# Optimization experiments

Hardware: AMD Instinct MI355X
Metric: run time of the kernel (lower is better)

## Reference

```python
import jax, jax.numpy as jnp
import numpy as np

N, F, H, D = 4096, 512, 4, 64        # nodes, in features, heads, per-head dim
HID, OUT, NCLS, E = 1024, 256, 40, 65536  # FFN hidden, GAT dim, classes, edges
EPS = 1e-5


def _bn(x, g, b):
    # BatchNorm1d with batch statistics (training-mode math, biased variance)
    m = x.mean(axis=0)
    v = jnp.var(x, axis=0)
    return (x - m) * jax.lax.rsqrt(v + EPS) * g + b


def _ffn(x, g1, b1, W1, c1, g2, b2, W2, c2):
    x = jax.nn.gelu(_bn(x, g1, b1) @ W1.T + c1, approximate=False)
    x = jax.nn.gelu(_bn(x, g2, b2) @ W2.T + c2, approximate=False)
    return x


def setup_inputs() -> dict:
    key = jax.random.key(0)
    ks = jax.random.split(key, 12)
    nrm = lambda k, shape: jax.random.normal(k, shape, jnp.float32) * 0.05
    node_features = jax.random.normal(ks[0], (N, F), jnp.float32)
    edges = jax.random.randint(ks[1], (2, E), 0, N)
    adj = jnp.eye(N, dtype=bool)  # self loops, as in __init__
    adj = adj.at[edges[0], edges[1]].set(True)
    adj = adj.at[edges[1], edges[0]].set(True)
    return dict(
        node_features=node_features,
        pre_g1=jnp.ones(F), pre_b1=jnp.zeros(F),
        pre_W1=nrm(ks[2], (HID, F)), pre_c1=jnp.zeros(HID),
        pre_g2=jnp.ones(HID), pre_b2=jnp.zeros(HID),
        pre_W2=nrm(ks[3], (OUT, HID)), pre_c2=jnp.zeros(OUT),
        Wp=nrm(ks[4], (H * D, OUT)),           # GAT preprocess Linear, no bias
        Wa=nrm(ks[5], (2 * D,)),               # attention Linear(2d -> 1), no bias
        ln_g=jnp.ones(OUT), ln_b=jnp.zeros(OUT),
        post_g1=jnp.ones(OUT), post_b1=jnp.zeros(OUT),
        post_W1=nrm(ks[6], (HID, OUT)), post_c1=jnp.zeros(HID),
        post_g2=jnp.ones(HID), post_b2=jnp.zeros(HID),
        post_W2=nrm(ks[7], (OUT, HID)), post_c2=jnp.zeros(OUT),
        Wl=nrm(ks[8], (NCLS, OUT)), cl=jnp.zeros(NCLS),
        adjacency=adj,
        input_node_indices=jax.random.randint(ks[9], (8192,), 0, N),
    )


def reference(node_features, pre_g1, pre_b1, pre_W1, pre_c1, pre_g2, pre_b2,
              pre_W2, pre_c2, Wp, Wa, ln_g, ln_b, post_g1, post_b1, post_W1,
              post_c1, post_g2, post_b2, post_W2, post_c2, Wl, cl,
              adjacency, input_node_indices):
    # preprocess FFN: [N,F] -> [N,OUT]
    x = _ffn(node_features, pre_g1, pre_b1, pre_W1, pre_c1,
             pre_g2, pre_b2, pre_W2, pre_c2)
    # GAT layer
    xh = (x @ Wp.T).reshape(N, H, D)
    # cat([x_source, x_target]) @ Wa == x[j] . Wa[:D] + x[i] . Wa[D:]
    a_src = jnp.einsum('jhd,d->jh', xh, Wa[:D])
    a_tgt = jnp.einsum('ihd,d->ih', xh, Wa[D:])
    e = jax.nn.leaky_relu(a_src[None, :, :] + a_tgt[:, None, :],
                          negative_slope=0.2)          # [i, j, h]
    e = jnp.where(adjacency[:, :, None], e, -jnp.inf)  # masked_fill(~adj, -inf)
    att = jax.nn.softmax(e, axis=1)                    # softmax over neighbors j
    h = jnp.einsum('ijh,jhd->ihd', att, xh).reshape(N, H * D)
    # residual + LayerNorm (dropout disabled for deterministic reference)
    x = x + h
    mu = x.mean(-1, keepdims=True)
    var = jnp.var(x, axis=-1, keepdims=True)
    x = (x - mu) * jax.lax.rsqrt(var + EPS) * ln_g + ln_b
    # postprocess FFN + gather + logits
    x = _ffn(x, post_g1, post_b1, post_W1, post_c1,
             post_g2, post_b2, post_W2, post_c2)
    emb = x[input_node_indices]
    return emb @ Wl.T + cl
```

## Files before the change

### kernel.cpp

```cpp
#include <hip/hip_runtime.h>
#include <hip/hip_bf16.h>


#define NNODES 4096
#define CAP 128

typedef unsigned short u16;
typedef __attribute__((ext_vector_type(8))) short bf16x8;
typedef __attribute__((ext_vector_type(4))) float f32x4;

__device__ __forceinline__ float gelu_f(float x) {
    return 0.5f * x * (1.0f + erff(x * 0.70710678118654752f));
}
__device__ __forceinline__ u16 f2bf(float x) {
    union { float f; unsigned u; } v; v.f = x;
    unsigned r = v.u + 0x7fff + ((v.u >> 16) & 1);
    return (u16)(r >> 16);
}
__device__ __forceinline__ float bf2f(u16 b) {
    return __uint_as_float(((unsigned)b) << 16);
}
__device__ __forceinline__ void gload16(const void* g, void* l) {
    __builtin_amdgcn_global_load_lds(
        (const __attribute__((address_space(1))) unsigned int*)g,
        (__attribute__((address_space(3))) unsigned int*)l, 16, 0, 0);
}

__global__ __launch_bounds__(256) void prep_kernel(
    const unsigned char* __restrict__ adj, int* __restrict__ nbr,
    int* __restrict__ deg, const float* __restrict__ nf,
    float* __restrict__ part, u16* __restrict__ nf16,
    const float* __restrict__ Wp, const float* __restrict__ Wl,
    const float* __restrict__ cl, u16* __restrict__ Wp16,
    u16* __restrict__ WlP16, float* __restrict__ CLP)
{
    __shared__ int lists[4][CAP];
    __shared__ int cnts[4];
    __shared__ int sflag;
    const int t = threadIdx.x;
    const int wv = t >> 6, lane = t & 63;

    if (blockIdx.x >= NNODES + 128) {
        const int n = blockIdx.x - (NNODES + 128);
        if (n < 256) {
            Wp16[(size_t)n * 256 + t] = f2bf(Wp[(size_t)n * 256 + t]);
        } else {
            int m = n - 256;
            if (m < 40) {
                WlP16[(size_t)m * 256 + t] = f2bf(Wl[(size_t)m * 256 + t]);
                if (t == 0) CLP[m] = cl[m];
            } else {
                WlP16[(size_t)m * 256 + t] = 0;
                if (t == 0) CLP[m] = 0.f;
            }
        }
        return;
    }

    if (blockIdx.x >= NNODES) {
        const int bid = blockIdx.x - NNODES;
        const int r0 = bid * 32;
        const int cchunk = t & 127;
        const int rsub = t >> 7;
        float s[4] = {0.f, 0.f, 0.f, 0.f}, q[4] = {0.f, 0.f, 0.f, 0.f};
        for (int r = rsub; r < 32; r += 2) {
            float4 v = *(const float4*)(nf + (size_t)(r0 + r) * 512 + cchunk * 4);
            float vv[4] = {v.x, v.y, v.z, v.w};
            ushort4 o;
            o.x = f2bf(vv[0]); o.y = f2bf(vv[1]);
            o.z = f2bf(vv[2]); o.w = f2bf(vv[3]);
            *(ushort4*)(nf16 + (size_t)(r0 + r) * 512 + cchunk * 4) = o;
#pragma unroll
            for (int j = 0; j < 4; ++j) { s[j] += vv[j]; q[j] += vv[j] * vv[j]; }
        }
        const size_t slice = (size_t)bid * 2 + rsub;
#pragma unroll
        for (int j = 0; j < 4; ++j) {
            int c = cchunk * 4 + j;
            part[(slice * 512 + c) * 2 + 0] = s[j];
            part[(slice * 512 + c) * 2 + 1] = q[j];
        }
        return;
    }

    const int i = blockIdx.x;
    if (wv == 0) {
        bool a = adj[(size_t)lane * 4097] != 0;
        bool b = ((const unsigned int*)adj)[(size_t)lane * 4097] != 0;
        unsigned long long mA = __ballot(a);
        unsigned long long mB = __ballot(b);
        if (lane == 0) sflag = (__popcll(mA) >= __popcll(mB)) ? 0 : 1;
    }
    __syncthreads();
    int cnt = 0;
    if (sflag == 1) {
        const uint4* row = (const uint4*)((const unsigned int*)adj + (size_t)i * NNODES);
#pragma unroll
        for (int w = 0; w < 4; ++w) {
            uint4 v = row[w * 256 + t];
            unsigned wd[4] = {v.x, v.y, v.z, v.w};
#pragma unroll
            for (int j = 0; j < 4; ++j) {
                bool on = wd[j] != 0;
                unsigned long long m = __ballot(on);
                int pre = __popcll(m & ((1ull << lane) - 1ull));
                if (on && cnt + pre < CAP)
                    lists[wv][cnt + pre] = (w * 256 + t) * 4 + j;
                cnt += __popcll(m);
            }
        }
    } else {
        uint4 v = ((const uint4*)(adj + (size_t)i * NNODES))[t];
        unsigned wd[4] = {v.x, v.y, v.z, v.w};
#pragma unroll
        for (int j = 0; j < 4; ++j)
#pragma unroll
            for (int b = 0; b < 4; ++b) {
                bool on = ((wd[j] >> (8 * b)) & 0xffu) != 0;
                unsigned long long m = __ballot(on);
                int pre = __popcll(m & ((1ull << lane) - 1ull));
                if (on && cnt + pre < CAP)
                    lists[wv][cnt + pre] = t * 16 + j * 4 + b;
                cnt += __popcll(m);
            }
    }
    if (lane == 0) cnts[wv] = cnt < CAP ? cnt : CAP;
    __syncthreads();
    int offw = 0;
#pragma unroll
    for (int w2 = 0; w2 < 4; ++w2) if (w2 < wv) offw += cnts[w2];
    int myc = cnts[wv];
    for (int k = lane; k < myc; k += 64) {
        int pos = offw + k;
        if (pos < CAP) nbr[(size_t)i * CAP + pos] = lists[wv][k];
    }
    if (t == 0) {
        int tot = cnts[0] + cnts[1] + cnts[2] + cnts[3];
        deg[i] = tot < CAP ? tot : CAP;
    }
}

__global__ __launch_bounds__(256) void xln_stats(
    const float* __restrict__ X, float* __restrict__ part)
{
    const int bid = blockIdx.x;
    const int r0 = bid * 32;
    const int t = threadIdx.x;
    const int cchunk = t & 63;
    const int rsub = t >> 6;
    float s[4] = {0.f, 0.f, 0.f, 0.f}, q[4] = {0.f, 0.f, 0.f, 0.f};
    for (int r = rsub; r < 32; r += 4) {
        float4 v = *(const float4*)(X + (size_t)(r0 + r) * 256 + cchunk * 4);
        float vv[4] = {v.x, v.y, v.z, v.w};
#pragma unroll
        for (int j = 0; j < 4; ++j) { s[j] += vv[j]; q[j] += vv[j] * vv[j]; }
    }
    const size_t slice = (size_t)bid * 4 + rsub;
#pragma unroll
    for (int j = 0; j < 4; ++j) {
        int c = cchunk * 4 + j;
        part[(slice * 256 + c) * 2 + 0] = s[j];
        part[(slice * 256 + c) * 2 + 1] = q[j];
    }
}

__global__ __launch_bounds__(256) void colstats_final(
    const float* __restrict__ part, const float* __restrict__ g,
    const float* __restrict__ bt, float* __restrict__ scl,
    float* __restrict__ shf, int NB, int C)
{
    __shared__ float sred[16][17];
    __shared__ float qred[16][17];
    const int t = threadIdx.x;
    const int cs = t & 15, grp = t >> 4;
    const int c = blockIdx.x * 16 + cs;
    float s = 0.f, q = 0.f;
    for (int b = grp; b < NB; b += 16) {
        s += part[((size_t)b * C + c) * 2 + 0];
        q += part[((size_t)b * C + c) * 2 + 1];
    }
    sred[grp][cs] = s; qred[grp][cs] = q;
    __syncthreads();
    if (grp == 0) {
        float S = 0.f, Q = 0.f;
#pragma unroll
        for (int j = 0; j < 16; ++j) { S += sred[j][cs]; Q += qred[j][cs]; }
        float m = S * (1.0f / 4096.0f);
        float v = Q * (1.0f / 4096.0f) - m * m;
        float sc = g[c] * rsqrtf(v + 1e-5f);
        scl[c] = sc;
        shf[c] = bt[c] - m * sc;
    }
}

__global__ __launch_bounds__(256) void foldw_kernel(
    const float* __restrict__ W, const float* __restrict__ scl,
    const float* __restrict__ shf, const float* __restrict__ bias,
    u16* __restrict__ W16, float* __restrict__ bout, int K, int nvalid)
{
    __shared__ float red[4];
    const int n = blockIdx.x, t = threadIdx.x;
    u16* o = W16 + (size_t)n * K;
    if (n >= nvalid) {
        for (int k = t; k < K; k += 256) o[k] = 0;
        if (t == 0) bout[n] = 0.f;
        return;
    }
    const float* w = W + (size_t)n * K;
    float part = 0.f;
    for (int k = t; k < K; k += 256) {
        float wv = w[k];
        float s = scl ? scl[k] : 1.f;
        float f = shf ? shf[k] : 0.f;
        o[k] = f2bf(wv * s);
        part += wv * f;
    }
    int lane = t & 63, wv_ = t >> 6;
#pragma unroll
    for (int off = 32; off > 0; off >>= 1) part += __shfl_down(part, off);
    if (lane == 0) red[wv_] = part;
    __syncthreads();
    if (t == 0)
        bout[n] = (bias ? bias[n] : 0.f) + red[0] + red[1] + red[2] + red[3];
}

template<bool EPI, bool S16, bool STATS>
__global__ __launch_bounds__(256) void mfma_gemm(
    const u16* __restrict__ A, const u16* __restrict__ W,
    const float* __restrict__ bias, u16* __restrict__ C16,
    float* __restrict__ PART, int M, int N, int K)
{
    __shared__ u16 As[2][4096];
    __shared__ u16 Bs[2][4096];
    __shared__ float ep1[2][64];
    __shared__ float ep2[2][64];
    const int t = threadIdx.x;
    const int lane = t & 63, wv = t >> 6;
    const int wm = (wv >> 1) * 32, wn = (wv & 1) * 32;
    const int tile_m = blockIdx.y * 64, tile_n = blockIdx.x * 64;

    f32x4 acc[2][2];
#pragma unroll
    for (int i = 0; i < 2; ++i)
#pragma unroll
        for (int j = 0; j < 2; ++j)
#pragma unroll
            for (int e = 0; e < 4; ++e) acc[i][j][e] = 0.f;

    int srow[2], soff[2];
#pragma unroll
    for (int i = 0; i < 2; ++i) {
        int f = i * 256 + t;
        srow[i] = f >> 3;
        soff[i] = ((f & 7) ^ (srow[i] & 7)) * 8;
    }
    const int wvoff = wv * 1024;
    const int frow_a0 = wm + (lane & 15);
    const int frow_b0 = wn + (lane & 15);
    const int fk = (lane >> 4) * 16;

    const int NT = K >> 6;
    int cur = 0;

#define STAGE(B, KT)                                                         \
    {                                                                        \
        _Pragma("unroll")                                                    \
        for (int i = 0; i < 2; ++i) {                                        \
            gload16(A + (size_t)(tile_m + srow[i]) * K + (KT) * 64 + soff[i],\
                    (char*)As[B] + wvoff + i * 4096);                        \
            gload16(W + (size_t)(tile_n + srow[i]) * K + (KT) * 64 + soff[i],\
                    (char*)Bs[B] + wvoff + i * 4096);                        \
        }                                                                    \
    }

    STAGE(0, 0);
    __syncthreads();
    for (int kt = 0; kt < NT; ++kt) {
        if (kt + 1 < NT) STAGE(cur ^ 1, kt + 1);
        const char* baseA = (const char*)As[cur];
        const char* baseB = (const char*)Bs[cur];
#pragma unroll
        for (int kk = 0; kk < 2; ++kk) {
            bf16x8 a[2], b[2];
#pragma unroll
            for (int mi = 0; mi < 2; ++mi) {
                int r = frow_a0 + mi * 16;
                a[mi] = *(const bf16x8*)(baseA + r * 128 +
                        ((kk * 64 + fk) ^ ((r & 7) << 4)));
            }
#pragma unroll
            for (int ni = 0; ni < 2; ++ni) {
                int r = frow_b0 + ni * 16;
                b[ni] = *(const bf16x8*)(baseB + r * 128 +
                        ((kk * 64 + fk) ^ ((r & 7) << 4)));
            }
#pragma unroll
            for (int mi = 0; mi < 2; ++mi)
#pragma unroll
                for (int ni = 0; ni < 2; ++ni)
                    acc[mi][ni] = __builtin_amdgcn_mfma_f32_16x16x32_bf16(
                        a[mi], b[ni], acc[mi][ni], 0, 0, 0);
        }
        __syncthreads();
        cur ^= 1;
    }
#undef STAGE

    float st0 = 0.f, st1 = 0.f, sq0 = 0.f, sq1 = 0.f;
#pragma unroll
    for (int mi = 0; mi < 2; ++mi) {
#pragma unroll
        for (int ni = 0; ni < 2; ++ni) {
            int col = tile_n + wn + ni * 16 + (lane & 15);
            float bs = 0.f;
            if (EPI) bs = bias[col];
#pragma unroll
            for (int e = 0; e < 4; ++e) {
                int row = tile_m + wm + mi * 16 + ((lane >> 4) << 2) + e;
                float c = acc[mi][ni][e];
                if (EPI) c = gelu_f(c + bs);
                if (S16) C16[(size_t)row * N + col] = f2bf(c);
                if (STATS) {
                    if (ni == 0) { st0 += c; sq0 += c * c; }
                    else         { st1 += c; sq1 += c * c; }
                }
            }
        }
    }

    if (STATS) {
        float s0 = st0, s1 = st1, q0 = sq0, q1 = sq1;
        s0 += __shfl_xor(s0, 16); s0 += __shfl_xor(s0, 32);
        s1 += __shfl_xor(s1, 16); s1 += __shfl_xor(s1, 32);
        q0 += __shfl_xor(q0, 16); q0 += __shfl_xor(q0, 32);
        q1 += __shfl_xor(q1, 16); q1 += __shfl_xor(q1, 32);
        if (lane < 16) {
            ep1[wv >> 1][wn + lane] = s0;       ep2[wv >> 1][wn + lane] = q0;
            ep1[wv >> 1][wn + 16 + lane] = s1;  ep2[wv >> 1][wn + 16 + lane] = q1;
        }
        __syncthreads();
        if (t < 64) {
            PART[((size_t)blockIdx.y * N + tile_n + t) * 2 + 0] = ep1[0][t] + ep1[1][t];
            PART[((size_t)blockIdx.y * N + tile_n + t) * 2 + 1] = ep2[0][t] + ep2[1][t];
        }
    }
}

template<bool EPI, bool S16, bool ASRCF>
__global__ __launch_bounds__(512) void mfma_gemm8(
    const u16* __restrict__ A, const u16* __restrict__ W,
    const float* __restrict__ bias, u16* __restrict__ C16,
    const float* __restrict__ Wa, float* __restrict__ ASRC,
    float* __restrict__ ATGT, int M, int N, int K)
{
    __shared__ u16 As[2][2][4096];
    __shared__ u16 Bs[2][2][4096];
    __shared__ float ep1[2][64];
    __shared__ float ep2[2][64];
    const int t = threadIdx.x;
    const int lane = t & 63, wv = t >> 6;
    const int kh = wv >> 2;
    const int wl = wv & 3;
    const int wm = (wl >> 1) * 32, wn = (wl & 1) * 32;
    const int tile_m = blockIdx.y * 64, tile_n = blockIdx.x * 64;

    f32x4 acc[2][2];
#pragma unroll
    for (int i = 0; i < 2; ++i)
#pragma unroll
        for (int j = 0; j < 2; ++j)
#pragma unroll
            for (int e = 0; e < 4; ++e) acc[i][j][e] = 0.f;

    const int ht = t & 255;
    int srow[2], soff[2];
#pragma unroll
    for (int i = 0; i < 2; ++i) {
        int f = i * 256 + ht;
        srow[i] = f >> 3;
        soff[i] = ((f & 7) ^ (srow[i] & 7)) * 8;
    }
    const int wvoff = wl * 1024;
    const int frow_a0 = wm + (lane & 15);
    const int frow_b0 = wn + (lane & 15);
    const int fk = (lane >> 4) * 16;

    const int NTh = (K >> 6) >> 1;
    const int kbase = kh * NTh;
    int cur = 0;

#define STAGE8(B, KT)                                                        \
    {                                                                        \
        _Pragma("unroll")                                                    \
        for (int i = 0; i < 2; ++i) {                                        \
            gload16(A + (size_t)(tile_m + srow[i]) * K + (kbase + (KT)) * 64 \
                        + soff[i],                                           \
                    (char*)As[B][kh] + wvoff + i * 4096);                    \
            gload16(W + (size_t)(tile_n + srow[i]) * K + (kbase + (KT)) * 64 \
                        + soff[i],                                           \
                    (char*)Bs[B][kh] + wvoff + i * 4096);                    \
        }                                                                    \
    }

    STAGE8(0, 0);
    __syncthreads();
    for (int kt = 0; kt < NTh; ++kt) {
        if (kt + 1 < NTh) STAGE8(cur ^ 1, kt + 1);
        const char* baseA = (const char*)As[cur][kh];
        const char* baseB = (const char*)Bs[cur][kh];
#pragma unroll
        for (int kk = 0; kk < 2; ++kk) {
            bf16x8 a[2], b[2];
#pragma unroll
            for (int mi = 0; mi < 2; ++mi) {
                int r = frow_a0 + mi * 16;
                a[mi] = *(const bf16x8*)(baseA + r * 128 +
                        ((kk * 64 + fk) ^ ((r & 7) << 4)));
            }
#pragma unroll
            for (int ni = 0; ni < 2; ++ni) {
                int r = frow_b0 + ni * 16;
                b[ni] = *(const bf16x8*)(baseB + r * 128 +
                        ((kk * 64 + fk) ^ ((r & 7) << 4)));
            }
#pragma unroll
            for (int mi = 0; mi < 2; ++mi)
#pragma unroll
                for (int ni = 0; ni < 2; ++ni)
                    acc[mi][ni] = __builtin_amdgcn_mfma_f32_16x16x32_bf16(
                        a[mi], b[ni], acc[mi][ni], 0, 0, 0);
        }
        __syncthreads();
        cur ^= 1;
    }
#undef STAGE8

    float* cb = (float*)&As[0][0][0];
    if (kh == 1) {
#pragma unroll
        for (int mi = 0; mi < 2; ++mi)
#pragma unroll
            for (int ni = 0; ni < 2; ++ni)
#pragma unroll
                for (int e = 0; e < 4; ++e)
                    cb[wl * 1024 + lane * 16 + (mi * 2 + ni) * 4 + e] =
                        acc[mi][ni][e];
    }
    __syncthreads();
    if (kh == 0) {
#pragma unroll
        for (int mi = 0; mi < 2; ++mi)
#pragma unroll
            for (int ni = 0; ni < 2; ++ni)
#pragma unroll
                for (int e = 0; e < 4; ++e)
                    acc[mi][ni][e] +=
                        cb[wl * 1024 + lane * 16 + (mi * 2 + ni) * 4 + e];

#pragma unroll
        for (int mi = 0; mi < 2; ++mi) {
#pragma unroll
            for (int ni = 0; ni < 2; ++ni) {
                int col = tile_n + wn + ni * 16 + (lane & 15);
                float bs = 0.f;
                if (EPI) bs = bias[col];
#pragma unroll
                for (int e = 0; e < 4; ++e) {
                    int row = tile_m + wm + mi * 16 + ((lane >> 4) << 2) + e;
                    float c = acc[mi][ni][e];
                    if (EPI) c = gelu_f(c + bs);
                    if (S16) C16[(size_t)row * N + col] = f2bf(c);
                }
            }
        }
    }

    if (ASRCF) {
        if (kh == 0) {
            const int cl = lane & 15;
            float ws0 = Wa[wn + cl],      ws1 = Wa[wn + 16 + cl];
            float wt0 = Wa[64 + wn + cl], wt1 = Wa[64 + wn + 16 + cl];
#pragma unroll
            for (int mi = 0; mi < 2; ++mi)
#pragma unroll
                for (int e = 0; e < 4; ++e) {
                    float vs = acc[mi][0][e] * ws0 + acc[mi][1][e] * ws1;
                    float vt = acc[mi][0][e] * wt0 + acc[mi][1][e] * wt1;
#pragma unroll
                    for (int off = 1; off < 16; off <<= 1) {
                        vs += __shfl_xor(vs, off);
                        vt += __shfl_xor(vt, off);
                    }
                    if (cl == 0) {
                        int row = wm + mi * 16 + ((lane >> 4) << 2) + e;
                        ep1[wl & 1][row] = vs;
                        ep2[wl & 1][row] = vt;
                    }
                }
        }
        __syncthreads();
        if (t < 64) {
            int head = blockIdx.x;
            ASRC[(size_t)(tile_m + t) * 4 + head] = ep1[0][t] + ep1[1][t];
            ATGT[(size_t)(tile_m + t) * 4 + head] = ep2[0][t] + ep2[1][t];
        }
    }
}

__global__ __launch_bounds__(512) void logits_mfma(
    const u16* __restrict__ xf16, const int* __restrict__ idxs,
    const u16* __restrict__ WlP, const float* __restrict__ clP,
    float* __restrict__ out)
{
    __shared__ u16 As[2][2][4096];
    __shared__ u16 Bs[2][2][4096];
    const int t = threadIdx.x;
    const int lane = t & 63, wv = t >> 6;
    const int kh = wv >> 2;
    const int wl = wv & 3;
    const int wm = (wl >> 1) * 32, wn = (wl & 1) * 32;
    const int tile_m = blockIdx.x * 64;

    f32x4 acc[2][2];
#pragma unroll
    for (int i = 0; i < 2; ++i)
#pragma unroll
        for (int j = 0; j < 2; ++j)
#pragma unroll
            for (int e = 0; e < 4; ++e) acc[i][j][e] = 0.f;

    const int ht = t & 255;
    int srow[2], soff[2], gr[2];
#pragma unroll
    for (int i = 0; i < 2; ++i) {
        int f = i * 256 + ht;
        srow[i] = f >> 3;
        soff[i] = ((f & 7) ^ (srow[i] & 7)) * 8;
        gr[i] = idxs[tile_m + srow[i]];
    }
    const int wvoff = wl * 1024;
    const int frow_a0 = wm + (lane & 15);
    const int frow_b0 = wn + (lane & 15);
    const int fk = (lane >> 4) * 16;
    const int kbase = kh * 2;

#define LSTAGE8(B, KT)                                                       \
    {                                                                        \
        _Pragma("unroll")                                                    \
        for (int i = 0; i < 2; ++i) {                                        \
            gload16(xf16 + (size_t)gr[i] * 256 + (kbase + (KT)) * 64         \
                        + soff[i],                                           \
                    (char*)As[B][kh] + wvoff + i * 4096);                    \
            gload16(WlP + (size_t)srow[i] * 256 + (kbase + (KT)) * 64        \
                        + soff[i],                                           \
                    (char*)Bs[B][kh] + wvoff + i * 4096);                    \
        }                                                                    \
    }

    int cur = 0;
    LSTAGE8(0, 0);
    __syncthreads();
#pragma unroll
    for (int kt = 0; kt < 2; ++kt) {
        if (kt + 1 < 2) LSTAGE8(cur ^ 1, kt + 1);
        const char* baseA = (const char*)As[cur][kh];
        const char* baseB = (const char*)Bs[cur][kh];
#pragma unroll
        for (int kk = 0; kk < 2; ++kk) {
            bf16x8 a[2], b[2];
#pragma unroll
            for (int mi = 0; mi < 2; ++mi) {
                int r = frow_a0 + mi * 16;
                a[mi] = *(const bf16x8*)(baseA + r * 128 +
                        ((kk * 64 + fk) ^ ((r & 7) << 4)));
            }
#pragma unroll
            for (int ni = 0; ni < 2; ++ni) {
                int r = frow_b0 + ni * 16;
                b[ni] = *(const bf16x8*)(baseB + r * 128 +
                        ((kk * 64 + fk) ^ ((r & 7) << 4)));
            }
#pragma unroll
            for (int mi = 0; mi < 2; ++mi)
#pragma unroll
                for (int ni = 0; ni < 2; ++ni)
                    acc[mi][ni] = __builtin_amdgcn_mfma_f32_16x16x32_bf16(
                        a[mi], b[ni], acc[mi][ni], 0, 0, 0);
        }
        __syncthreads();
        cur ^= 1;
    }
#undef LSTAGE8

    float* cb = (float*)&As[0][0][0];
    if (kh == 1) {
#pragma unroll
        for (int mi = 0; mi < 2; ++mi)
#pragma unroll
            for (int ni = 0; ni < 2; ++ni)
#pragma unroll
                for (int e = 0; e < 4; ++e)
                    cb[wl * 1024 + lane * 16 + (mi * 2 + ni) * 4 + e] =
                        acc[mi][ni][e];
    }
    __syncthreads();
    if (kh == 0) {
#pragma unroll
        for (int mi = 0; mi < 2; ++mi) {
#pragma unroll
            for (int ni = 0; ni < 2; ++ni) {
                int col = wn + ni * 16 + (lane & 15);
                float cbsum0 = cb[wl * 1024 + lane * 16 + (mi * 2 + ni) * 4];
                (void)cbsum0;
                if (col < 40) {
                    float bs = clP[col];
#pragma unroll
                    for (int e = 0; e < 4; ++e) {
                        int row = tile_m + wm + mi * 16 + ((lane >> 4) << 2) + e;
                        float c = acc[mi][ni][e] +
                            cb[wl * 1024 + lane * 16 + (mi * 2 + ni) * 4 + e];
                        out[(size_t)row * 40 + col] = c + bs;
                    }
                }
            }
        }
    }
}

__global__ __launch_bounds__(256) void attn_ln_kernel(
    const u16* __restrict__ xh, const u16* __restrict__ x0,
    const float* __restrict__ asrc, const float* __restrict__ atgt,
    const int* __restrict__ nbr, const int* __restrict__ deg_,
    const float* __restrict__ ln_g, const float* __restrict__ ln_b,
    float* __restrict__ xln32, u16* __restrict__ xln16)
{
    __shared__ float att[CAP * 4];
    __shared__ int nb[CAP];
    __shared__ float red[8];
    const int i = blockIdx.x;
    const int t = threadIdx.x;
    const int wv = t >> 6, lane = t & 63;
    const int dg = deg_[i];

    for (int k = t; k < dg; k += 256) nb[k] = nbr[(size_t)i * CAP + k];
    __syncthreads();

    for (int idx = t; idx < dg * 4; idx += 256) {
        int k = idx >> 2, h = idx & 3;
        float e = asrc[nb[k] * 4 + h] + atgt[i * 4 + h];
        att[idx] = e > 0.f ? e : 0.2f * e;
    }
    __syncthreads();

    {
        const int h = wv;
        float m = -1e30f;
        for (int k = lane; k < dg; k += 64) m = fmaxf(m, att[k * 4 + h]);
#pragma unroll
        for (int off = 32; off > 0; off >>= 1) m = fmaxf(m, __shfl_xor(m, off));
        float s = 0.f;
        for (int k = lane; k < dg; k += 64) s += expf(att[k * 4 + h] - m);
#pragma unroll
        for (int off = 32; off > 0; off >>= 1) s += __shfl_xor(s, off);
        float inv = 1.0f / s;
        for (int k = lane; k < dg; k += 64)
            att[k * 4 + h] = expf(att[k * 4 + h] - m) * inv;
    }

    const int h = wv;
    float acc = 0.f;
    int k = 0;
    for (; k + 4 <= dg; k += 4) {
        float a0 = att[(k + 0) * 4 + h], v0 = bf2f(xh[(size_t)nb[k + 0] * 256 + t]);
        float a1 = att[(k + 1) * 4 + h], v1 = bf2f(xh[(size_t)nb[k + 1] * 256 + t]);
        float a2 = att[(k + 2) * 4 + h], v2 = bf2f(xh[(size_t)nb[k + 2] * 256 + t]);
        float a3 = att[(k + 3) * 4 + h], v3 = bf2f(xh[(size_t)nb[k + 3] * 256 + t]);
        acc = fmaf(a0, v0, acc); acc = fmaf(a1, v1, acc);
        acc = fmaf(a2, v2, acc); acc = fmaf(a3, v3, acc);
    }
    for (; k < dg; ++k)
        acc = fmaf(att[k * 4 + h], bf2f(xh[(size_t)nb[k] * 256 + t]), acc);

    float v = bf2f(x0[(size_t)i * 256 + t]) + acc;
    float s = v, q = v * v;
#pragma unroll
    for (int off = 32; off > 0; off >>= 1) {
        s += __shfl_xor(s, off);
        q += __shfl_xor(q, off);
    }
    if (lane == 0) { red[wv] = s; red[4 + wv] = q; }
    __syncthreads();
    float S = red[0] + red[1] + red[2] + red[3];
    float Q = red[4] + red[5] + red[6] + red[7];
    float mu = S * (1.0f / 256.0f);
    float var = Q * (1.0f / 256.0f) - mu * mu;
    float y = (v - mu) * rsqrtf(var + 1e-5f) * ln_g[t] + ln_b[t];
    xln32[(size_t)i * 256 + t] = y;
    xln16[(size_t)i * 256 + t] = f2bf(y);
}

extern "C" void kernel_launch(void* const* d_in, const int* in_sizes, int n_in,
                              void* d_out, int out_size, void* d_ws, size_t ws_size,
                              hipStream_t stream)
{
    const float* nf      = (const float*)d_in[0];
    const float* pre_g1  = (const float*)d_in[1];
    const float* pre_b1  = (const float*)d_in[2];
    const float* pre_W1  = (const float*)d_in[3];
    const float* pre_c1  = (const float*)d_in[4];
    const float* pre_g2  = (const float*)d_in[5];
    const float* pre_b2  = (const float*)d_in[6];
    const float* pre_W2  = (const float*)d_in[7];
    const float* pre_c2  = (const float*)d_in[8];
    const float* Wp      = (const float*)d_in[9];
    const float* Wa      = (const float*)d_in[10];
    const float* ln_g    = (const float*)d_in[11];
    const float* ln_b    = (const float*)d_in[12];
    const float* post_g1 = (const float*)d_in[13];
    const float* post_b1 = (const float*)d_in[14];
    const float* post_W1 = (const float*)d_in[15];
    const float* post_c1 = (const float*)d_in[16];
    const float* post_g2 = (const float*)d_in[17];
    const float* post_b2 = (const float*)d_in[18];
    const float* post_W2 = (const float*)d_in[19];
    const float* post_c2 = (const float*)d_in[20];
    const float* Wl      = (const float*)d_in[21];
    const float* cl      = (const float*)d_in[22];
    const unsigned char* adj = (const unsigned char*)d_in[23];
    const int* idxs      = (const int*)d_in[24];
    float* out = (float*)d_out;

    size_t off = 0;
    char* base = (char*)d_ws;
    auto carve = [&](size_t bytes) {
        void* p = base + off;
        off += (bytes + 255) & ~(size_t)255;
        return p;
    };
    u16*   Y16   = (u16*)  carve((size_t)4096 * 1024 * 2);
    u16*   NF16  = (u16*)  carve((size_t)4096 * 512 * 2);
    u16*   X016  = (u16*)  carve((size_t)4096 * 256 * 2);
    u16*   XH16  = (u16*)  carve((size_t)4096 * 256 * 2);
    float* XLN32 = (float*)carve((size_t)4096 * 256 * 4);
    u16*   XLN16 = (u16*)  carve((size_t)4096 * 256 * 2);
    u16*   XF16  = (u16*)  carve((size_t)4096 * 256 * 2);
    u16*   W1_16 = (u16*)  carve((size_t)1024 * 512 * 2);
    u16*   W2_16 = (u16*)  carve((size_t)256 * 1024 * 2);
    u16*   Wp16  = (u16*)  carve((size_t)256 * 256 * 2);
    u16*   W3_16 = (u16*)  carve((size_t)1024 * 256 * 2);
    u16*   W4_16 = (u16*)  carve((size_t)256 * 1024 * 2);
    u16*   WlP16 = (u16*)  carve((size_t)64 * 256 * 2);
    float* B1    = (float*)carve(1024 * 4);
    float* B2    = (float*)carve(256 * 4);
    float* B3    = (float*)carve(1024 * 4);
    float* B4    = (float*)carve(256 * 4);
    float* CLP   = (float*)carve(64 * 4);
    int*   NBR   = (int*)  carve((size_t)4096 * CAP * 4);
    int*   DEG   = (int*)  carve((size_t)4096 * 4);
    float* ASRC  = (float*)carve((size_t)4096 * 4 * 4);
    float* ATGT  = (float*)carve((size_t)4096 * 4 * 4);
    float* PART  = (float*)carve((size_t)512 * 512 * 2 * 4);
    float* SCL1  = (float*)carve(512 * 4);
    float* SHF1  = (float*)carve(512 * 4);
    float* SCL2  = (float*)carve(1024 * 4);
    float* SHF2  = (float*)carve(1024 * 4);
    float* SCL3  = (float*)carve(256 * 4);
    float* SHF3  = (float*)carve(256 * 4);
    float* SCL4  = (float*)carve(1024 * 4);
    float* SHF4  = (float*)carve(1024 * 4);
    (void)ws_size; (void)n_in; (void)in_sizes; (void)out_size;

    prep_kernel<<<NNODES + 128 + 320, 256, 0, stream>>>(
        adj, NBR, DEG, nf, PART, NF16, Wp, Wl, cl, Wp16, WlP16, CLP);

    colstats_final<<<512 / 16, 256, 0, stream>>>(PART, pre_g1, pre_b1, SCL1, SHF1, 256, 512);
    foldw_kernel<<<1024, 256, 0, stream>>>(pre_W1, SCL1, SHF1, pre_c1, W1_16, B1, 512, 1024);
    mfma_gemm<true, true, true><<<dim3(16, 64), 256, 0, stream>>>(
        NF16, W1_16, B1, Y16, PART, 4096, 1024, 512);

    colstats_final<<<1024 / 16, 256, 0, stream>>>(PART, pre_g2, pre_b2, SCL2, SHF2, 64, 1024);
    foldw_kernel<<<256, 256, 0, stream>>>(pre_W2, SCL2, SHF2, pre_c2, W2_16, B2, 1024, 256);
    mfma_gemm8<true, true, false><<<dim3(4, 64), 512, 0, stream>>>(
        Y16, W2_16, B2, X016, nullptr, nullptr, nullptr, 4096, 256, 1024);

    mfma_gemm8<false, true, true><<<dim3(4, 64), 512, 0, stream>>>(
        X016, Wp16, nullptr, XH16, Wa, ASRC, ATGT, 4096, 256, 256);

    attn_ln_kernel<<<4096, 256, 0, stream>>>(XH16, X016, ASRC, ATGT, NBR, DEG,
                                             ln_g, ln_b, XLN32, XLN16);

    xln_stats<<<128, 256, 0, stream>>>(XLN32, PART);
    colstats_final<<<256 / 16, 256, 0, stream>>>(PART, post_g1, post_b1, SCL3, SHF3, 512, 256);
    foldw_kernel<<<1024, 256, 0, stream>>>(post_W1, SCL3, SHF3, post_c1, W3_16, B3, 256, 1024);
    mfma_gemm<true, true, true><<<dim3(16, 64), 256, 0, stream>>>(
        XLN16, W3_16, B3, Y16, PART, 4096, 1024, 256);

    colstats_final<<<1024 / 16, 256, 0, stream>>>(PART, post_g2, post_b2, SCL4, SHF4, 64, 1024);
    foldw_kernel<<<256, 256, 0, stream>>>(post_W2, SCL4, SHF4, post_c2, W4_16, B4, 1024, 256);
    mfma_gemm8<true, true, false><<<dim3(4, 64), 512, 0, stream>>>(
        Y16, W4_16, B4, XF16, nullptr, nullptr, nullptr, 4096, 256, 1024);

    logits_mfma<<<128, 512, 0, stream>>>(XF16, idxs, WlP16, CLP, out);
}
```

Baseline: 135.6 us.

## Fuse BN column-stat finalization into weight folding and shrink partial-sum count

Merges the colstats_final and foldw kernels into one foldbn_kernel. Each block recomputes the per-column BN scale and shift from the partial sums into shared memory, then folds them into several weight rows. The stats producers now reduce more rows per block and sum their sub-slices in shared memory, so 64 partial slices are written instead of 128-512. This removes four kernel launches and the scale/shift round trip through global memory. In exchange, every fold block redundantly reads all partials, and the number of blocks in the fold kernels drops.

```diff
diff --git a/kernel.cpp b/kernel.cpp
--- a/kernel.cpp
+++ b/kernel.cpp
@@ -37,11 +37,13 @@
     __shared__ int lists[4][CAP];
     __shared__ int cnts[4];
     __shared__ int sflag;
+    __shared__ float sb[2][512];
+    __shared__ float qb[2][512];
     const int t = threadIdx.x;
     const int wv = t >> 6, lane = t & 63;
 
-    if (blockIdx.x >= NNODES + 128) {
-        const int n = blockIdx.x - (NNODES + 128);
+    if (blockIdx.x >= NNODES + 64) {
+        const int n = blockIdx.x - (NNODES + 64);
         if (n < 256) {
             Wp16[(size_t)n * 256 + t] = f2bf(Wp[(size_t)n * 256 + t]);
         } else {
@@ -59,11 +61,11 @@
 
     if (blockIdx.x >= NNODES) {
         const int bid = blockIdx.x - NNODES;
-        const int r0 = bid * 32;
+        const int r0 = bid * 64;
         const int cchunk = t & 127;
         const int rsub = t >> 7;
         float s[4] = {0.f, 0.f, 0.f, 0.f}, q[4] = {0.f, 0.f, 0.f, 0.f};
-        for (int r = rsub; r < 32; r += 2) {
+        for (int r = rsub; r < 64; r += 2) {
             float4 v = *(const float4*)(nf + (size_t)(r0 + r) * 512 + cchunk * 4);
             float vv[4] = {v.x, v.y, v.z, v.w};
             ushort4 o;
@@ -73,12 +75,19 @@
 #pragma unroll
             for (int j = 0; j < 4; ++j) { s[j] += vv[j]; q[j] += vv[j] * vv[j]; }
         }
-        const size_t slice = (size_t)bid * 2 + rsub;
 #pragma unroll
         for (int j = 0; j < 4; ++j) {
-            int c = cchunk * 4 + j;
-            part[(slice * 512 + c) * 2 + 0] = s[j];
-            part[(slice * 512 + c) * 2 + 1] = q[j];
+            sb[rsub][cchunk * 4 + j] = s[j];
+            qb[rsub][cchunk * 4 + j] = q[j];
+        }
+        __syncthreads();
+        if (rsub == 0) {
+#pragma unroll
+            for (int j = 0; j < 4; ++j) {
+                int c = cchunk * 4 + j;
+                part[((size_t)bid * 512 + c) * 2 + 0] = sb[0][c] + sb[1][c];
+                part[((size_t)bid * 512 + c) * 2 + 1] = qb[0][c] + qb[1][c];
+            }
         }
         return;
     }
@@ -143,85 +152,97 @@
 __global__ __launch_bounds__(256) void xln_stats(
     const float* __restrict__ X, float* __restrict__ part)
 {
+    __shared__ float sb[4][256];
+    __shared__ float qb[4][256];
     const int bid = blockIdx.x;
-    const int r0 = bid * 32;
+    const int r0 = bid * 64;
     const int t = threadIdx.x;
     const int cchunk = t & 63;
     const int rsub = t >> 6;
     float s[4] = {0.f, 0.f, 0.f, 0.f}, q[4] = {0.f, 0.f, 0.f, 0.f};
-    for (int r = rsub; r < 32; r += 4) {
+    for (int r = rsub; r < 64; r += 4) {
         float4 v = *(const float4*)(X + (size_t)(r0 + r) * 256 + cchunk * 4);
         float vv[4] = {v.x, v.y, v.z, v.w};
 #pragma unroll
         for (int j = 0; j < 4; ++j) { s[j] += vv[j]; q[j] += vv[j] * vv[j]; }
     }
-    const size_t slice = (size_t)bid * 4 + rsub;
 #pragma unroll
     for (int j = 0; j < 4; ++j) {
-        int c = cchunk * 4 + j;
-        part[(slice * 256 + c) * 2 + 0] = s[j];
-        part[(slice * 256 + c) * 2 + 1] = q[j];
-    }
-}
-
-__global__ __launch_bounds__(256) void colstats_final(
-    const float* __restrict__ part, const float* __restrict__ g,
-    const float* __restrict__ bt, float* __restrict__ scl,
-    float* __restrict__ shf, int NB, int C)
+        sb[rsub][cchunk * 4 + j] = s[j];
+        qb[rsub][cchunk * 4 + j] = q[j];
+    }
+    __syncthreads();
+    if (t < 64) {
+#pragma unroll
+        for (int j = 0; j < 4; ++j) {
+            int c = t * 4 + j;
+            part[((size_t)bid * 256 + c) * 2 + 0] =
+                sb[0][c] + sb[1][c] + sb[2][c] + sb[3][c];
+            part[((size_t)bid * 256 + c) * 2 + 1] =
+                qb[0][c] + qb[1][c] + qb[2][c] + qb[3][c];
+        }
+    }
+}
+
+template<int C, int RPB>
+__global__ __launch_bounds__(256) void foldbn_kernel(
+    const float* __restrict__ PART, const float* __restrict__ g,
+    const float* __restrict__ bt, const float* __restrict__ W,
+    const float* __restrict__ bias, u16* __restrict__ W16,
+    float* __restrict__ bout)
 {
-    __shared__ float sred[16][17];
-    __shared__ float qred[16][17];
+    constexpr int CPT = C / 256;
+    __shared__ float scl_s[C];
+    __shared__ float shf_s[C];
+    __shared__ float redL[RPB][4];
     const int t = threadIdx.x;
-    const int cs = t & 15, grp = t >> 4;
-    const int c = blockIdx.x * 16 + cs;
-    float s = 0.f, q = 0.f;
-    for (int b = grp; b < NB; b += 16) {
-        s += part[((size_t)b * C + c) * 2 + 0];
-        q += part[((size_t)b * C + c) * 2 + 1];
-    }
-    sred[grp][cs] = s; qred[grp][cs] = q;
-    __syncthreads();
-    if (grp == 0) {
-        float S = 0.f, Q = 0.f;
-#pragma unroll
-        for (int j = 0; j < 16; ++j) { S += sred[j][cs]; Q += qred[j][cs]; }
-        float m = S * (1.0f / 4096.0f);
-        float v = Q * (1.0f / 4096.0f) - m * m;
-        float sc = g[c] * rsqrtf(v + 1e-5f);
-        scl[c] = sc;
-        shf[c] = bt[c] - m * sc;
-    }
-}
-
-__global__ __launch_bounds__(256) void foldw_kernel(
-    const float* __restrict__ W, const float* __restrict__ scl,
-    const float* __restrict__ shf, const float* __restrict__ bias,
-    u16* __restrict__ W16, float* __restrict__ bout, int K, int nvalid)
-{
-    __shared__ float red[4];
-    const int n = blockIdx.x, t = threadIdx.x;
-    u16* o = W16 + (size_t)n * K;
-    if (n >= nvalid) {
-        for (int k = t; k < K; k += 256) o[k] = 0;
-        if (t == 0) bout[n] = 0.f;
-        return;
-    }
-    const float* w = W + (size_t)n * K;
-    float part = 0.f;
-    for (int k = t; k < K; k += 256) {
-        float wv = w[k];
-        float s = scl ? scl[k] : 1.f;
-        float f = shf ? shf[k] : 0.f;
-        o[k] = f2bf(wv * s);
-        part += wv * f;
-    }
-    int lane = t & 63, wv_ = t >> 6;
-#pragma unroll
-    for (int off = 32; off > 0; off >>= 1) part += __shfl_down(part, off);
-    if (lane == 0) red[wv_] = part;
-    __syncthreads();
-    if (t == 0)
-        bout[n] = (bias ? bias[n] : 0.f) + red[0] + red[1] + red[2] + red[3];
+    const int lane = t & 63, wv_ = t >> 6;
+
+    {
+        float s[CPT], q[CPT];
+#pragma unroll
+        for (int j = 0; j < CPT; ++j) { s[j] = 0.f; q[j] = 0.f; }
+        const int c0 = t * CPT;
+        for (int b = 0; b < 64; ++b) {
+            const float* p = PART + ((size_t)b * C + c0) * 2;
+#pragma unroll
+            for (int j = 0; j < CPT; ++j) {
+                s[j] += p[j * 2 + 0];
+                q[j] += p[j * 2 + 1];
+            }
+        }
+#pragma unroll
+        for (int j = 0; j < CPT; ++j) {
+            int c = c0 + j;
+            float m = s[j] * (1.0f / 4096.0f);
+            float v = q[j] * (1.0f / 4096.0f) - m * m;
+            float sc = g[c] * rsqrtf(v + 1e-5f);
+            scl_s[c] = sc;
+            shf_s[c] = bt[c] - m * sc;
+        }
+    }
+    __syncthreads();
+
+#pragma unroll
+    for (int rr = 0; rr < RPB; ++rr) {
+        int n = blockIdx.x * RPB + rr;
+        const float* w = W + (size_t)n * C;
+        u16* o = W16 + (size_t)n * C;
+        float part = 0.f;
+        for (int k = t; k < C; k += 256) {
+            float wv = w[k];
+            o[k] = f2bf(wv * scl_s[k]);
+            part += wv * shf_s[k];
+        }
+#pragma unroll
+        for (int off = 32; off > 0; off >>= 1) part += __shfl_down(part, off);
+        if (lane == 0) redL[rr][wv_] = part;
+    }
+    __syncthreads();
+    if (t < RPB) {
+        int n = blockIdx.x * RPB + t;
+        bout[n] = bias[n] + redL[t][0] + redL[t][1] + redL[t][2] + redL[t][3];
+    }
 }
 
 template<bool EPI, bool S16, bool STATS>
@@ -610,8 +631,6 @@
 #pragma unroll
             for (int ni = 0; ni < 2; ++ni) {
                 int col = wn + ni * 16 + (lane & 15);
-                float cbsum0 = cb[wl * 1024 + lane * 16 + (mi * 2 + ni) * 4];
-                (void)cbsum0;
                 if (col < 40) {
                     float bs = clP[col];
 #pragma unroll
@@ -759,27 +778,19 @@
     int*   DEG   = (int*)  carve((size_t)4096 * 4);
     float* ASRC  = (float*)carve((size_t)4096 * 4 * 4);
     float* ATGT  = (float*)carve((size_t)4096 * 4 * 4);
-    float* PART  = (float*)carve((size_t)512 * 512 * 2 * 4);
-    float* SCL1  = (float*)carve(512 * 4);
-    float* SHF1  = (float*)carve(512 * 4);
-    float* SCL2  = (float*)carve(1024 * 4);
-    float* SHF2  = (float*)carve(1024 * 4);
-    float* SCL3  = (float*)carve(256 * 4);
-    float* SHF3  = (float*)carve(256 * 4);
-    float* SCL4  = (float*)carve(1024 * 4);
-    float* SHF4  = (float*)carve(1024 * 4);
+    float* PART  = (float*)carve((size_t)64 * 1024 * 2 * 4);
     (void)ws_size; (void)n_in; (void)in_sizes; (void)out_size;
 
-    prep_kernel<<<NNODES + 128 + 320, 256, 0, stream>>>(
+    prep_kernel<<<NNODES + 64 + 320, 256, 0, stream>>>(
         adj, NBR, DEG, nf, PART, NF16, Wp, Wl, cl, Wp16, WlP16, CLP);
 
-    colstats_final<<<512 / 16, 256, 0, stream>>>(PART, pre_g1, pre_b1, SCL1, SHF1, 256, 512);
-    foldw_kernel<<<1024, 256, 0, stream>>>(pre_W1, SCL1, SHF1, pre_c1, W1_16, B1, 512, 1024);
+    foldbn_kernel<512, 4><<<256, 256, 0, stream>>>(
+        PART, pre_g1, pre_b1, pre_W1, pre_c1, W1_16, B1);
     mfma_gemm<true, true, true><<<dim3(16, 64), 256, 0, stream>>>(
         NF16, W1_16, B1, Y16, PART, 4096, 1024, 512);
 
-    colstats_final<<<1024 / 16, 256, 0, stream>>>(PART, pre_g2, pre_b2, SCL2, SHF2, 64, 1024);
-    foldw_kernel<<<256, 256, 0, stream>>>(pre_W2, SCL2, SHF2, pre_c2, W2_16, B2, 1024, 256);
+    foldbn_kernel<1024, 2><<<128, 256, 0, stream>>>(
+        PART, pre_g2, pre_b2, pre_W2, pre_c2, W2_16, B2);
     mfma_gemm8<true, true, false><<<dim3(4, 64), 512, 0, stream>>>(
         Y16, W2_16, B2, X016, nullptr, nullptr, nullptr, 4096, 256, 1024);
 
@@ -789,14 +800,14 @@
     attn_ln_kernel<<<4096, 256, 0, stream>>>(XH16, X016, ASRC, ATGT, NBR, DEG,
                                              ln_g, ln_b, XLN32, XLN16);
 
-    xln_stats<<<128, 256, 0, stream>>>(XLN32, PART);
-    colstats_final<<<256 / 16, 256, 0, stream>>>(PART, post_g1, post_b1, SCL3, SHF3, 512, 256);
-    foldw_kernel<<<1024, 256, 0, stream>>>(post_W1, SCL3, SHF3, post_c1, W3_16, B3, 256, 1024);
+    xln_stats<<<64, 256, 0, stream>>>(XLN32, PART);
+    foldbn_kernel<256, 4><<<256, 256, 0, stream>>>(
+        PART, post_g1, post_b1, post_W1, post_c1, W3_16, B3);
     mfma_gemm<true, true, true><<<dim3(16, 64), 256, 0, stream>>>(
         XLN16, W3_16, B3, Y16, PART, 4096, 1024, 256);
 
-    colstats_final<<<1024 / 16, 256, 0, stream>>>(PART, post_g2, post_b2, SCL4, SHF4, 64, 1024);
-    foldw_kernel<<<256, 256, 0, stream>>>(post_W2, SCL4, SHF4, post_c2, W4_16, B4, 1024, 256);
+    foldbn_kernel<1024, 2><<<128, 256, 0, stream>>>(
+        PART, post_g2, post_b2, post_W2, post_c2, W4_16, B4);
     mfma_gemm8<true, true, false><<<dim3(4, 64), 512, 0, stream>>>(
         Y16, W4_16, B4, XF16, nullptr, nullptr, nullptr, 4096, 256, 1024);
 
```

Result: slower. 143.5 us (+5.8%).
